# Kernel optimization log

Measured on AMD Instinct MI355X. Metric: run time of the kernel, lower is better.

The kernel has to match this reference:

```python
import jax, jax.numpy as jnp
import numpy as np

N = 4096      # nodes
F = 128       # input feature dim
HEADS = 8     # attention_num
U = 8         # units per head


def setup_inputs() -> dict:
    key = jax.random.key(0)
    k_a, k_h, k_w, k_al, k_ar = jax.random.split(key, 5)
    A = jax.random.randint(k_a, (N, N), 0, 2).astype(jnp.float32)   # dense 0/1 adjacency
    H = jax.random.normal(k_h, (N, F), dtype=jnp.float32)
    W = jax.random.normal(k_w, (HEADS, F, U), dtype=jnp.float32) * 0.1
    a_left = jax.random.normal(k_al, (HEADS, U), dtype=jnp.float32) * 0.1
    a_right = jax.random.normal(k_ar, (HEADS, U), dtype=jnp.float32) * 0.1
    return {"A": A, "H": H, "W": W, "a_left": a_left, "a_right": a_right}


def reference(A, H, W, a_left, a_right):
    # Per-head attention logits: E[h,i,j] = e_left[h,i] + e_right[h,j]
    e_l = jnp.einsum('nf,hfu,hu->hn', H, W, a_left)    # [HEADS, N]
    e_r = jnp.einsum('nf,hfu,hu->hn', H, W, a_right)   # [HEADS, N]
    E = e_l[:, :, None] + e_r[:, None, :]              # [HEADS, N, N]
    # Faithful to original: denominator uses exp(E * A) (zeros in A -> exp(0)=1)
    denom = jnp.sum(jnp.exp(E * A[None]), axis=-1, keepdims=True)   # [HEADS, N, 1]
    Alpha = jnp.exp(E) / denom * A[None]               # masked attention weights
    # Aggregate then project: elu(Alpha @ H @ W) per head
    out = jax.nn.elu(jnp.einsum('hij,jf,hfu->hiu', Alpha, H, W))    # [HEADS, N, U]
    # is_output_layer=False -> concat heads along feature dim: [N, HEADS*U]
    return jnp.transpose(out, (1, 0, 2)).reshape(H.shape[0], HEADS * U)
```

## Files before the change

kernel.cpp:

```cpp
#include <hip/hip_runtime.h>
#include <hip/hip_bf16.h>

#define NN 4096
#define FF 128
#define NC 80
#define LSTR 84

typedef __attribute__((ext_vector_type(4))) float float4v;
typedef __attribute__((ext_vector_type(4))) unsigned int uint4v;
typedef __attribute__((ext_vector_type(8))) short short8;

static __device__ inline unsigned short bfb(float x) {
    __hip_bfloat16 b = __float2bfloat16(x);
    return *(unsigned short*)&b;
}
static __device__ inline float bff(unsigned short u) {
    __hip_bfloat16 b = *(__hip_bfloat16*)&u;
    return __bfloat162float(b);
}

__global__ __launch_bounds__(256) void gat_wsplit(const float* __restrict__ W,
                                                  const float* __restrict__ al,
                                                  const float* __restrict__ ar,
                                                  __hip_bfloat16* __restrict__ Wphi,
                                                  __hip_bfloat16* __restrict__ Wplo)
{
    const int tid = blockIdx.x * 256 + threadIdx.x;
    if (tid >= 80 * FF) return;
    const int c = tid % 80;
    const int f = tid / 80;
    float val;
    if (c < 64) {
        val = W[(size_t)(c >> 3) * (FF * 8) + (size_t)f * 8 + (c & 7)];
    } else {
        const int hc = (c - 64) & 7;
        const float* ap = (c < 72) ? ar : al;
        const float* wp = W + (size_t)hc * (FF * 8) + (size_t)f * 8;
        float s = 0.f;
        #pragma unroll
        for (int u = 0; u < 8; ++u) s += wp[u] * ap[hc * 8 + u];
        val = s;
    }
    const unsigned short h = bfb(val);
    const unsigned short l = bfb(val - bff(h));
    const int g = (f >> 5) * 4 + ((f >> 3) & 3);
    const size_t idx = ((size_t)g * NC + c) * 8 + (f & 7);
    Wphi[idx] = *(const __hip_bfloat16*)&h;
    Wplo[idx] = *(const __hip_bfloat16*)&l;
}

__global__ __launch_bounds__(256) void gat_prep(const float* __restrict__ H,
                                                const __hip_bfloat16* __restrict__ Wphi,
                                                const __hip_bfloat16* __restrict__ Wplo,
                                                float* __restrict__ expEl,
                                                __hip_bfloat16* __restrict__ Bp)
{
    __shared__ float Lp[4 * 16 * LSTR];
    const int t    = threadIdx.x;
    const int wave = t >> 6;
    const int lane = t & 63;
    const int j0   = blockIdx.x * 16;
    const int m16  = lane & 15, q = lane >> 4;
    const short* Whs = (const short*)Wphi;
    const short* Wls = (const short*)Wplo;
    const int kt = wave;

    const float* hp = H + (size_t)(j0 + m16) * FF + kt * 32 + q * 8;
    float4v x0 = *(const float4v*)hp;
    float4v x1 = *(const float4v*)(hp + 4);
    short8 ahi, alo;
    #pragma unroll
    for (int i = 0; i < 4; ++i) {
        const unsigned short h0 = bfb(x0[i]);
        ahi[i] = (short)h0;
        alo[i] = (short)bfb(x0[i] - bff(h0));
        const unsigned short h1 = bfb(x1[i]);
        ahi[4 + i] = (short)h1;
        alo[4 + i] = (short)bfb(x1[i] - bff(h1));
    }

    const short8* bh = (const short8*)(Whs + (size_t)(kt * 4 + q) * NC * 8);
    const short8* bl = (const short8*)(Wls + (size_t)(kt * 4 + q) * NC * 8);
    float4v acc[5] = {};
    #pragma unroll
    for (int nt = 0; nt < 5; ++nt) {
        short8 bhi = bh[nt * 16 + m16];
        short8 blo = bl[nt * 16 + m16];
        acc[nt] = __builtin_amdgcn_mfma_f32_16x16x32_bf16(ahi, bhi, acc[nt], 0, 0, 0);
        acc[nt] = __builtin_amdgcn_mfma_f32_16x16x32_bf16(alo, bhi, acc[nt], 0, 0, 0);
        acc[nt] = __builtin_amdgcn_mfma_f32_16x16x32_bf16(ahi, blo, acc[nt], 0, 0, 0);
    }

    float* Lw = Lp + wave * (16 * LSTR);
    #pragma unroll
    for (int nt = 0; nt < 5; ++nt) {
        #pragma unroll
        for (int r = 0; r < 4; ++r)
            Lw[(q * 4 + r) * LSTR + nt * 16 + m16] = acc[nt][r];
    }
    __syncthreads();

    const int jl = t >> 4, g = t & 15;
    const float* Lr = Lp + jl * LSTR;
    const int jg = j0 + jl;
    const size_t base = ((size_t)((jg >> 5) * 4 + ((jg >> 3) & 3)) * NC) * 8 + (jg & 7);

    #pragma unroll
    for (int i = 0; i < 4; ++i) {
        const int c = g + 16 * i;
        const int h = (g >> 3) + 2 * i;
        const float er = expf(Lr[64 + h] + Lr[16 * LSTR + 64 + h] +
                              Lr[32 * LSTR + 64 + h] + Lr[48 * LSTR + 64 + h]);
        const float v = Lr[c] + Lr[16 * LSTR + c] +
                        Lr[32 * LSTR + c] + Lr[48 * LSTR + c];
        Bp[base + (size_t)c * 8] = __float2bfloat16(er * v);
    }
    float v64;
    if (g < 8) {
        v64 = expf(Lr[64 + g] + Lr[16 * LSTR + 64 + g] +
                   Lr[32 * LSTR + 64 + g] + Lr[48 * LSTR + 64 + g]);
    } else {
        v64 = (g == 8) ? 1.0f : 0.0f;
    }
    Bp[base + (size_t)(64 + g) * 8] = __float2bfloat16(v64);
    if (g >= 8) {
        const int h = g - 8;
        expEl[h * NN + jg] = expf(Lr[72 + h] + Lr[16 * LSTR + 72 + h] +
                                  Lr[32 * LSTR + 72 + h] + Lr[48 * LSTR + 72 + h]);
    }
}

__global__ __launch_bounds__(512) void gat_gemm(const float* __restrict__ A,
                                                const __hip_bfloat16* __restrict__ Bp,
                                                const float* __restrict__ expEl,
                                                float* __restrict__ out)
{
    __shared__ float Ls[8 * 16 * LSTR];
    const int rb   = blockIdx.x;
    const int wave = threadIdx.x >> 6;
    const int lane = threadIdx.x & 63;
    const int m16  = lane & 15;
    const int q    = lane >> 4;
    const int row0 = rb * 16;

    float4v acc[5] = {};

    const int k0 = wave * 512;
    const unsigned int* Au = (const unsigned int*)A;
    const short8* bb = (const short8*)Bp;
    const unsigned int* arow = Au + (size_t)(row0 + m16) * NN + q * 8 + k0;

    const size_t bw = (size_t)(wave * 16) * 4 * NC + (size_t)q * NC + (size_t)m16;

    uint4v a0[4], a1[4];
    #pragma unroll
    for (int i = 0; i < 4; ++i) {
        a0[i] = *(const uint4v*)(arow + i * 32);
        a1[i] = *(const uint4v*)(arow + i * 32 + 4);
    }
    short8 bbuf[2][5];
    #pragma unroll
    for (int nt = 0; nt < 5; ++nt)
        bbuf[0][nt] = bb[bw + (size_t)nt * 16];

    #pragma unroll
    for (int kt = 0; kt < 16; ++kt) {
        const int cur = kt & 3;
        const int pb  = kt & 1, nb = pb ^ 1;

        if (kt + 1 < 16) {
            #pragma unroll
            for (int nt = 0; nt < 5; ++nt)
                bbuf[nb][nt] = bb[bw + (size_t)(kt + 1) * (4 * NC) + (size_t)nt * 16];
        }

        short8 afrag;
        afrag[0] = (short)(a0[cur][0] >> 16); afrag[1] = (short)(a0[cur][1] >> 16);
        afrag[2] = (short)(a0[cur][2] >> 16); afrag[3] = (short)(a0[cur][3] >> 16);
        afrag[4] = (short)(a1[cur][0] >> 16); afrag[5] = (short)(a1[cur][1] >> 16);
        afrag[6] = (short)(a1[cur][2] >> 16); afrag[7] = (short)(a1[cur][3] >> 16);

        if (kt + 4 < 16) {
            a0[cur] = *(const uint4v*)(arow + (kt + 4) * 32);
            a1[cur] = *(const uint4v*)(arow + (kt + 4) * 32 + 4);
        }

        #pragma unroll
        for (int nt = 0; nt < 5; ++nt)
            acc[nt] = __builtin_amdgcn_mfma_f32_16x16x32_bf16(afrag, bbuf[pb][nt], acc[nt], 0, 0, 0);
    }

    float* Lw = Ls + wave * (16 * LSTR);
    #pragma unroll
    for (int nt = 0; nt < 5; ++nt) {
        #pragma unroll
        for (int r = 0; r < 4; ++r)
            Lw[(q * 4 + r) * LSTR + nt * 16 + m16] = acc[nt][r];
    }
    __syncthreads();

    #pragma unroll
    for (int p = threadIdx.x; p < 1024; p += 512) {
        const int il = p >> 6;
        const int c  = p & 63;
        const int h  = c >> 3;
        float T = 0.f, S = 0.f, dg = 0.f;
        #pragma unroll
        for (int w = 0; w < 8; ++w) {
            const float* rowp = Ls + w * (16 * LSTR) + il * LSTR;
            T  += rowp[c];
            S  += rowp[64 + h];
            dg += rowp[72];
        }
        const float el = expEl[h * NN + row0 + il];
        const float denom = ((float)NN - dg) + el * S;
        const float x = el * T / denom;
        out[(size_t)(row0 + il) * 64 + c] = x > 0.f ? x : expf(x) - 1.f;
    }
}

extern "C" void kernel_launch(void* const* d_in, const int* in_sizes, int n_in,
                              void* d_out, int out_size, void* d_ws, size_t ws_size,
                              hipStream_t stream) {
    const float* A  = (const float*)d_in[0];
    const float* H  = (const float*)d_in[1];
    const float* W  = (const float*)d_in[2];
    const float* al = (const float*)d_in[3];
    const float* ar = (const float*)d_in[4];
    float* out = (float*)d_out;

    float* expEl = (float*)d_ws;
    __hip_bfloat16* Bp   = (__hip_bfloat16*)((char*)d_ws + 131072);
    __hip_bfloat16* Wphi = (__hip_bfloat16*)((char*)d_ws + 131072 + 655360);
    __hip_bfloat16* Wplo = (__hip_bfloat16*)((char*)d_ws + 131072 + 655360 + 20480);

    gat_wsplit<<<40, 256, 0, stream>>>(W, al, ar, Wphi, Wplo);
    gat_prep<<<NN / 16, 256, 0, stream>>>(H, Wphi, Wplo, expEl, Bp);
    gat_gemm<<<NN / 16, 512, 0, stream>>>(A, Bp, expEl, out);
}
```

Measured before the change: 118.2 us.

## Fuse three GAT kernels into one cooperative kernel with grid syncs

Merges the weight-split, feature-projection and adjacency GEMM kernels into a single cooperative launch of 256 blocks of 512 threads, using grid-wide syncs between stages. This removes two kernel-launch gaps and their inter-kernel idle time. In exchange it adds grid barrier overhead, idles half the threads in the prep stage, and relies on all 256 blocks being co-resident.

```diff
diff --git a/kernel.cpp b/kernel.cpp
--- a/kernel.cpp
+++ b/kernel.cpp
@@ -1,5 +1,8 @@
 #include <hip/hip_runtime.h>
 #include <hip/hip_bf16.h>
+#include <hip/hip_cooperative_groups.h>
+
+namespace cg = cooperative_groups;
 
 #define NN 4096
 #define FF 128
@@ -19,203 +22,212 @@
     return __bfloat162float(b);
 }
 
-__global__ __launch_bounds__(256) void gat_wsplit(const float* __restrict__ W,
-                                                  const float* __restrict__ al,
-                                                  const float* __restrict__ ar,
-                                                  __hip_bfloat16* __restrict__ Wphi,
-                                                  __hip_bfloat16* __restrict__ Wplo)
-{
-    const int tid = blockIdx.x * 256 + threadIdx.x;
-    if (tid >= 80 * FF) return;
-    const int c = tid % 80;
-    const int f = tid / 80;
-    float val;
-    if (c < 64) {
-        val = W[(size_t)(c >> 3) * (FF * 8) + (size_t)f * 8 + (c & 7)];
-    } else {
-        const int hc = (c - 64) & 7;
-        const float* ap = (c < 72) ? ar : al;
-        const float* wp = W + (size_t)hc * (FF * 8) + (size_t)f * 8;
-        float s = 0.f;
-        #pragma unroll
-        for (int u = 0; u < 8; ++u) s += wp[u] * ap[hc * 8 + u];
-        val = s;
-    }
-    const unsigned short h = bfb(val);
-    const unsigned short l = bfb(val - bff(h));
-    const int g = (f >> 5) * 4 + ((f >> 3) & 3);
-    const size_t idx = ((size_t)g * NC + c) * 8 + (f & 7);
-    Wphi[idx] = *(const __hip_bfloat16*)&h;
-    Wplo[idx] = *(const __hip_bfloat16*)&l;
-}
-
-__global__ __launch_bounds__(256) void gat_prep(const float* __restrict__ H,
-                                                const __hip_bfloat16* __restrict__ Wphi,
-                                                const __hip_bfloat16* __restrict__ Wplo,
-                                                float* __restrict__ expEl,
-                                                __hip_bfloat16* __restrict__ Bp)
-{
-    __shared__ float Lp[4 * 16 * LSTR];
-    const int t    = threadIdx.x;
-    const int wave = t >> 6;
-    const int lane = t & 63;
-    const int j0   = blockIdx.x * 16;
-    const int m16  = lane & 15, q = lane >> 4;
-    const short* Whs = (const short*)Wphi;
-    const short* Wls = (const short*)Wplo;
-    const int kt = wave;
-
-    const float* hp = H + (size_t)(j0 + m16) * FF + kt * 32 + q * 8;
-    float4v x0 = *(const float4v*)hp;
-    float4v x1 = *(const float4v*)(hp + 4);
-    short8 ahi, alo;
-    #pragma unroll
-    for (int i = 0; i < 4; ++i) {
-        const unsigned short h0 = bfb(x0[i]);
-        ahi[i] = (short)h0;
-        alo[i] = (short)bfb(x0[i] - bff(h0));
-        const unsigned short h1 = bfb(x1[i]);
-        ahi[4 + i] = (short)h1;
-        alo[4 + i] = (short)bfb(x1[i] - bff(h1));
-    }
-
-    const short8* bh = (const short8*)(Whs + (size_t)(kt * 4 + q) * NC * 8);
-    const short8* bl = (const short8*)(Wls + (size_t)(kt * 4 + q) * NC * 8);
-    float4v acc[5] = {};
-    #pragma unroll
-    for (int nt = 0; nt < 5; ++nt) {
-        short8 bhi = bh[nt * 16 + m16];
-        short8 blo = bl[nt * 16 + m16];
-        acc[nt] = __builtin_amdgcn_mfma_f32_16x16x32_bf16(ahi, bhi, acc[nt], 0, 0, 0);
-        acc[nt] = __builtin_amdgcn_mfma_f32_16x16x32_bf16(alo, bhi, acc[nt], 0, 0, 0);
-        acc[nt] = __builtin_amdgcn_mfma_f32_16x16x32_bf16(ahi, blo, acc[nt], 0, 0, 0);
-    }
-
-    float* Lw = Lp + wave * (16 * LSTR);
-    #pragma unroll
-    for (int nt = 0; nt < 5; ++nt) {
-        #pragma unroll
-        for (int r = 0; r < 4; ++r)
-            Lw[(q * 4 + r) * LSTR + nt * 16 + m16] = acc[nt][r];
-    }
-    __syncthreads();
-
-    const int jl = t >> 4, g = t & 15;
-    const float* Lr = Lp + jl * LSTR;
-    const int jg = j0 + jl;
-    const size_t base = ((size_t)((jg >> 5) * 4 + ((jg >> 3) & 3)) * NC) * 8 + (jg & 7);
-
-    #pragma unroll
-    for (int i = 0; i < 4; ++i) {
-        const int c = g + 16 * i;
-        const int h = (g >> 3) + 2 * i;
-        const float er = expf(Lr[64 + h] + Lr[16 * LSTR + 64 + h] +
-                              Lr[32 * LSTR + 64 + h] + Lr[48 * LSTR + 64 + h]);
-        const float v = Lr[c] + Lr[16 * LSTR + c] +
-                        Lr[32 * LSTR + c] + Lr[48 * LSTR + c];
-        Bp[base + (size_t)c * 8] = __float2bfloat16(er * v);
-    }
-    float v64;
-    if (g < 8) {
-        v64 = expf(Lr[64 + g] + Lr[16 * LSTR + 64 + g] +
-                   Lr[32 * LSTR + 64 + g] + Lr[48 * LSTR + 64 + g]);
-    } else {
-        v64 = (g == 8) ? 1.0f : 0.0f;
-    }
-    Bp[base + (size_t)(64 + g) * 8] = __float2bfloat16(v64);
-    if (g >= 8) {
-        const int h = g - 8;
-        expEl[h * NN + jg] = expf(Lr[72 + h] + Lr[16 * LSTR + 72 + h] +
-                                  Lr[32 * LSTR + 72 + h] + Lr[48 * LSTR + 72 + h]);
-    }
-}
-
-__global__ __launch_bounds__(512) void gat_gemm(const float* __restrict__ A,
-                                                const __hip_bfloat16* __restrict__ Bp,
-                                                const float* __restrict__ expEl,
-                                                float* __restrict__ out)
+__global__ __launch_bounds__(512) void gat_fused(const float* __restrict__ A,
+                                                 const float* __restrict__ H,
+                                                 const float* __restrict__ W,
+                                                 const float* __restrict__ al,
+                                                 const float* __restrict__ ar,
+                                                 float* __restrict__ expEl,
+                                                 __hip_bfloat16* __restrict__ Bp,
+                                                 __hip_bfloat16* __restrict__ Wphi,
+                                                 __hip_bfloat16* __restrict__ Wplo,
+                                                 float* __restrict__ out)
 {
     __shared__ float Ls[8 * 16 * LSTR];
-    const int rb   = blockIdx.x;
-    const int wave = threadIdx.x >> 6;
-    const int lane = threadIdx.x & 63;
-    const int m16  = lane & 15;
-    const int q    = lane >> 4;
-    const int row0 = rb * 16;
-
-    float4v acc[5] = {};
-
-    const int k0 = wave * 512;
-    const unsigned int* Au = (const unsigned int*)A;
-    const short8* bb = (const short8*)Bp;
-    const unsigned int* arow = Au + (size_t)(row0 + m16) * NN + q * 8 + k0;
-
-    const size_t bw = (size_t)(wave * 16) * 4 * NC + (size_t)q * NC + (size_t)m16;
-
-    uint4v a0[4], a1[4];
-    #pragma unroll
-    for (int i = 0; i < 4; ++i) {
-        a0[i] = *(const uint4v*)(arow + i * 32);
-        a1[i] = *(const uint4v*)(arow + i * 32 + 4);
+    cg::grid_group grid = cg::this_grid();
+
+    {
+        const int tid = blockIdx.x * 512 + threadIdx.x;
+        if (tid < 80 * FF) {
+            const int c = tid % 80;
+            const int f = tid / 80;
+            float val;
+            if (c < 64) {
+                val = W[(size_t)(c >> 3) * (FF * 8) + (size_t)f * 8 + (c & 7)];
+            } else {
+                const int hc = (c - 64) & 7;
+                const float* ap = (c < 72) ? ar : al;
+                const float* wp = W + (size_t)hc * (FF * 8) + (size_t)f * 8;
+                float s = 0.f;
+                #pragma unroll
+                for (int u = 0; u < 8; ++u) s += wp[u] * ap[hc * 8 + u];
+                val = s;
+            }
+            const unsigned short h = bfb(val);
+            const unsigned short l = bfb(val - bff(h));
+            const int g = (f >> 5) * 4 + ((f >> 3) & 3);
+            const size_t idx = ((size_t)g * NC + c) * 8 + (f & 7);
+            Wphi[idx] = *(const __hip_bfloat16*)&h;
+            Wplo[idx] = *(const __hip_bfloat16*)&l;
+        }
     }
-    short8 bbuf[2][5];
-    #pragma unroll
-    for (int nt = 0; nt < 5; ++nt)
-        bbuf[0][nt] = bb[bw + (size_t)nt * 16];
-
-    #pragma unroll
-    for (int kt = 0; kt < 16; ++kt) {
-        const int cur = kt & 3;
-        const int pb  = kt & 1, nb = pb ^ 1;
-
-        if (kt + 1 < 16) {
+    __threadfence();
+    grid.sync();
+
+    {
+        const int t = threadIdx.x;
+        if (t < 256) {
+            const int wave = t >> 6;
+            const int lane = t & 63;
+            const int j0   = blockIdx.x * 16;
+            const int m16  = lane & 15, q = lane >> 4;
+            const short* Whs = (const short*)Wphi;
+            const short* Wls = (const short*)Wplo;
+            const int kt = wave;
+
+            const float* hp = H + (size_t)(j0 + m16) * FF + kt * 32 + q * 8;
+            float4v x0 = *(const float4v*)hp;
+            float4v x1 = *(const float4v*)(hp + 4);
+            short8 ahi, alo;
+            #pragma unroll
+            for (int i = 0; i < 4; ++i) {
+                const unsigned short h0 = bfb(x0[i]);
+                ahi[i] = (short)h0;
+                alo[i] = (short)bfb(x0[i] - bff(h0));
+                const unsigned short h1 = bfb(x1[i]);
+                ahi[4 + i] = (short)h1;
+                alo[4 + i] = (short)bfb(x1[i] - bff(h1));
+            }
+
+            const short8* bh = (const short8*)(Whs + (size_t)(kt * 4 + q) * NC * 8);
+            const short8* bl = (const short8*)(Wls + (size_t)(kt * 4 + q) * NC * 8);
+            float4v acc[5] = {};
+            #pragma unroll
+            for (int nt = 0; nt < 5; ++nt) {
+                short8 bhi = bh[nt * 16 + m16];
+                short8 blo = bl[nt * 16 + m16];
+                acc[nt] = __builtin_amdgcn_mfma_f32_16x16x32_bf16(ahi, bhi, acc[nt], 0, 0, 0);
+                acc[nt] = __builtin_amdgcn_mfma_f32_16x16x32_bf16(alo, bhi, acc[nt], 0, 0, 0);
+                acc[nt] = __builtin_amdgcn_mfma_f32_16x16x32_bf16(ahi, blo, acc[nt], 0, 0, 0);
+            }
+
+            float* Lw = Ls + wave * (16 * LSTR);
+            #pragma unroll
+            for (int nt = 0; nt < 5; ++nt) {
+                #pragma unroll
+                for (int r = 0; r < 4; ++r)
+                    Lw[(q * 4 + r) * LSTR + nt * 16 + m16] = acc[nt][r];
+            }
+        }
+        __syncthreads();
+        if (t < 256) {
+            const int jl = t >> 4, g = t & 15;
+            const int j0 = blockIdx.x * 16;
+            const float* Lr = Ls + jl * LSTR;
+            const int jg = j0 + jl;
+            const size_t base = ((size_t)((jg >> 5) * 4 + ((jg >> 3) & 3)) * NC) * 8 + (jg & 7);
+
+            #pragma unroll
+            for (int i = 0; i < 4; ++i) {
+                const int c = g + 16 * i;
+                const int h = (g >> 3) + 2 * i;
+                const float er = expf(Lr[64 + h] + Lr[16 * LSTR + 64 + h] +
+                                      Lr[32 * LSTR + 64 + h] + Lr[48 * LSTR + 64 + h]);
+                const float v = Lr[c] + Lr[16 * LSTR + c] +
+                                Lr[32 * LSTR + c] + Lr[48 * LSTR + c];
+                Bp[base + (size_t)c * 8] = __float2bfloat16(er * v);
+            }
+            float v64;
+            if (g < 8) {
+                v64 = expf(Lr[64 + g] + Lr[16 * LSTR + 64 + g] +
+                           Lr[32 * LSTR + 64 + g] + Lr[48 * LSTR + 64 + g]);
+            } else {
+                v64 = (g == 8) ? 1.0f : 0.0f;
+            }
+            Bp[base + (size_t)(64 + g) * 8] = __float2bfloat16(v64);
+            if (g >= 8) {
+                const int h = g - 8;
+                expEl[h * NN + jg] = expf(Lr[72 + h] + Lr[16 * LSTR + 72 + h] +
+                                          Lr[32 * LSTR + 72 + h] + Lr[48 * LSTR + 72 + h]);
+            }
+        }
+    }
+    __threadfence();
+    grid.sync();
+    __syncthreads();
+
+    {
+        const int rb   = blockIdx.x;
+        const int wave = threadIdx.x >> 6;
+        const int lane = threadIdx.x & 63;
+        const int m16  = lane & 15;
+        const int q    = lane >> 4;
+        const int row0 = rb * 16;
+
+        float4v acc[5] = {};
+
+        const int k0 = wave * 512;
+        const unsigned int* Au = (const unsigned int*)A;
+        const short8* bb = (const short8*)Bp;
+        const unsigned int* arow = Au + (size_t)(row0 + m16) * NN + q * 8 + k0;
+
+        const size_t bw = (size_t)(wave * 16) * 4 * NC + (size_t)q * NC + (size_t)m16;
+
+        uint4v a0[4], a1[4];
+        #pragma unroll
+        for (int i = 0; i < 4; ++i) {
+            a0[i] = *(const uint4v*)(arow + i * 32);
+            a1[i] = *(const uint4v*)(arow + i * 32 + 4);
+        }
+        short8 bbuf[2][5];
+        #pragma unroll
+        for (int nt = 0; nt < 5; ++nt)
+            bbuf[0][nt] = bb[bw + (size_t)nt * 16];
+
+        #pragma unroll
+        for (int kt = 0; kt < 16; ++kt) {
+            const int cur = kt & 3;
+            const int pb  = kt & 1, nb = pb ^ 1;
+
+            if (kt + 1 < 16) {
+                #pragma unroll
+                for (int nt = 0; nt < 5; ++nt)
+                    bbuf[nb][nt] = bb[bw + (size_t)(kt + 1) * (4 * NC) + (size_t)nt * 16];
+            }
+
+            short8 afrag;
+            afrag[0] = (short)(a0[cur][0] >> 16); afrag[1] = (short)(a0[cur][1] >> 16);
+            afrag[2] = (short)(a0[cur][2] >> 16); afrag[3] = (short)(a0[cur][3] >> 16);
+            afrag[4] = (short)(a1[cur][0] >> 16); afrag[5] = (short)(a1[cur][1] >> 16);
+            afrag[6] = (short)(a1[cur][2] >> 16); afrag[7] = (short)(a1[cur][3] >> 16);
+
+            if (kt + 4 < 16) {
+                a0[cur] = *(const uint4v*)(arow + (kt + 4) * 32);
+                a1[cur] = *(const uint4v*)(arow + (kt + 4) * 32 + 4);
+            }
+
             #pragma unroll
             for (int nt = 0; nt < 5; ++nt)
-                bbuf[nb][nt] = bb[bw + (size_t)(kt + 1) * (4 * NC) + (size_t)nt * 16];
-        }
-
-        short8 afrag;
-        afrag[0] = (short)(a0[cur][0] >> 16); afrag[1] = (short)(a0[cur][1] >> 16);
-        afrag[2] = (short)(a0[cur][2] >> 16); afrag[3] = (short)(a0[cur][3] >> 16);
-        afrag[4] = (short)(a1[cur][0] >> 16); afrag[5] = (short)(a1[cur][1] >> 16);
-        afrag[6] = (short)(a1[cur][2] >> 16); afrag[7] = (short)(a1[cur][3] >> 16);
-
-        if (kt + 4 < 16) {
-            a0[cur] = *(const uint4v*)(arow + (kt + 4) * 32);
-            a1[cur] = *(const uint4v*)(arow + (kt + 4) * 32 + 4);
-        }
-
-        #pragma unroll
-        for (int nt = 0; nt < 5; ++nt)
-            acc[nt] = __builtin_amdgcn_mfma_f32_16x16x32_bf16(afrag, bbuf[pb][nt], acc[nt], 0, 0, 0);
-    }
-
-    float* Lw = Ls + wave * (16 * LSTR);
-    #pragma unroll
-    for (int nt = 0; nt < 5; ++nt) {
-        #pragma unroll
-        for (int r = 0; r < 4; ++r)
-            Lw[(q * 4 + r) * LSTR + nt * 16 + m16] = acc[nt][r];
-    }
-    __syncthreads();
-
-    #pragma unroll
-    for (int p = threadIdx.x; p < 1024; p += 512) {
-        const int il = p >> 6;
-        const int c  = p & 63;
-        const int h  = c >> 3;
-        float T = 0.f, S = 0.f, dg = 0.f;
-        #pragma unroll
-        for (int w = 0; w < 8; ++w) {
-            const float* rowp = Ls + w * (16 * LSTR) + il * LSTR;
-            T  += rowp[c];
-            S  += rowp[64 + h];
-            dg += rowp[72];
-        }
-        const float el = expEl[h * NN + row0 + il];
-        const float denom = ((float)NN - dg) + el * S;
-        const float x = el * T / denom;
-        out[(size_t)(row0 + il) * 64 + c] = x > 0.f ? x : expf(x) - 1.f;
+                acc[nt] = __builtin_amdgcn_mfma_f32_16x16x32_bf16(afrag, bbuf[pb][nt], acc[nt], 0, 0, 0);
+        }
+
+        float* Lw = Ls + wave * (16 * LSTR);
+        #pragma unroll
+        for (int nt = 0; nt < 5; ++nt) {
+            #pragma unroll
+            for (int r = 0; r < 4; ++r)
+                Lw[(q * 4 + r) * LSTR + nt * 16 + m16] = acc[nt][r];
+        }
+        __syncthreads();
+
+        #pragma unroll
+        for (int p = threadIdx.x; p < 1024; p += 512) {
+            const int il = p >> 6;
+            const int c  = p & 63;
+            const int h  = c >> 3;
+            float T = 0.f, S = 0.f, dg = 0.f;
+            #pragma unroll
+            for (int w = 0; w < 8; ++w) {
+                const float* rowp = Ls + w * (16 * LSTR) + il * LSTR;
+                T  += rowp[c];
+                S  += rowp[64 + h];
+                dg += rowp[72];
+            }
+            const float el = expEl[h * NN + row0 + il];
+            const float denom = ((float)NN - dg) + el * S;
+            const float x = el * T / denom;
+            out[(size_t)(row0 + il) * 64 + c] = x > 0.f ? x : expf(x) - 1.f;
+        }
     }
 }
 
@@ -234,7 +246,7 @@
     __hip_bfloat16* Wphi = (__hip_bfloat16*)((char*)d_ws + 131072 + 655360);
     __hip_bfloat16* Wplo = (__hip_bfloat16*)((char*)d_ws + 131072 + 655360 + 20480);
 
-    gat_wsplit<<<40, 256, 0, stream>>>(W, al, ar, Wphi, Wplo);
-    gat_prep<<<NN / 16, 256, 0, stream>>>(H, Wphi, Wplo, expEl, Bp);
-    gat_gemm<<<NN / 16, 512, 0, stream>>>(A, Bp, expEl, out);
-}
+    void* args[] = {(void*)&A, (void*)&H, (void*)&W, (void*)&al, (void*)&ar,
+                    (void*)&expEl, (void*)&Bp, (void*)&Wphi, (void*)&Wplo, (void*)&out};
+    hipLaunchCooperativeKernel((void*)gat_fused, dim3(256), dim3(512), args, 0, stream);
+}
```

Measured after the change: 250.3 us. 112% more time.
